# Performance work log

Hardware: AMD Instinct MI355X
Metric: run time of the kernel (lower is better)

The kernel has to match this reference:

```python
import jax, jax.numpy as jnp
import numpy as np

B, T, I, H, NC = 128, 256, 512, 1024, 1


def setup_inputs() -> dict:
    key = jax.random.key(0)
    ks = jax.random.split(key, 11)
    s = 1.0 / np.sqrt(H)  # torch nn.LSTM default init scale
    return {
        "x": jax.random.normal(ks[0], (B, T, I), jnp.float32),
        "W_ih0": jax.random.normal(ks[1], (4 * H, I), jnp.float32) * s,
        "W_hh0": jax.random.normal(ks[2], (4 * H, H), jnp.float32) * s,
        "b_ih0": jax.random.normal(ks[3], (4 * H,), jnp.float32) * s,
        "b_hh0": jax.random.normal(ks[4], (4 * H,), jnp.float32) * s,
        "W_ih1": jax.random.normal(ks[5], (4 * H, H), jnp.float32) * s,
        "W_hh1": jax.random.normal(ks[6], (4 * H, H), jnp.float32) * s,
        "b_ih1": jax.random.normal(ks[7], (4 * H,), jnp.float32) * s,
        "b_hh1": jax.random.normal(ks[8], (4 * H,), jnp.float32) * s,
        "W_fc": jax.random.normal(ks[9], (NC, H), jnp.float32) * s,
        "b_fc": jax.random.normal(ks[10], (NC,), jnp.float32) * s,
    }


def _lstm_layer(x_seq, W_ih, W_hh, b_ih, b_hh):
    # x_seq: [B, T, F]; torch gate order: i, f, g, o along 4H axis.
    b, h = x_seq.shape[0], W_hh.shape[1]
    # Precompute input projections for all timesteps (one big GEMM).
    x_proj = jnp.einsum("btf,gf->btg", x_seq, W_ih) + b_ih + b_hh  # [B,T,4H]

    def step(carry, xg):
        hprev, cprev = carry
        gates = xg + hprev @ W_hh.T  # [B,4H]
        i, f, g, o = jnp.split(gates, 4, axis=-1)
        c = jax.nn.sigmoid(f) * cprev + jax.nn.sigmoid(i) * jnp.tanh(g)
        hnew = jax.nn.sigmoid(o) * jnp.tanh(c)
        return (hnew, c), hnew

    init = (jnp.zeros((b, h), x_seq.dtype), jnp.zeros((b, h), x_seq.dtype))
    _, hs = jax.lax.scan(step, init, jnp.swapaxes(x_proj, 0, 1))  # [T,B,H]
    return jnp.swapaxes(hs, 0, 1)  # [B,T,H]


def reference(x, W_ih0, W_hh0, b_ih0, b_hh0, W_ih1, W_hh1, b_ih1, b_hh1, W_fc, b_fc):
    h1 = _lstm_layer(x, W_ih0, W_hh0, b_ih0, b_hh0)
    h2 = _lstm_layer(h1, W_ih1, W_hh1, b_ih1, b_hh1)
    return h2[:, -1, :] @ W_fc.T + b_fc  # [B, num_classes]
```

## Files before the change

kernel.cpp:

```cpp
#include <hip/hip_runtime.h>
#include <math.h>

typedef _Float16 half_t;
typedef _Float16 half8 __attribute__((ext_vector_type(8)));
typedef float f32x4 __attribute__((ext_vector_type(4)));
typedef unsigned long long u64;

#define B_ 128
#define T_ 256
#define I_ 512
#define H_ 1024

#define mfma16 __builtin_amdgcn_mfma_f32_16x16x32_f16

__global__ void k_convert_x(const float* __restrict__ x, half_t* __restrict__ x16, int n8) {
    int i = blockIdx.x * blockDim.x + threadIdx.x;
    if (i >= n8) return;
    const float4* xv = (const float4*)x;
    float4 a = xv[2 * i], b = xv[2 * i + 1];
    half8 o;
    o[0] = (half_t)a.x; o[1] = (half_t)a.y; o[2] = (half_t)a.z; o[3] = (half_t)a.w;
    o[4] = (half_t)b.x; o[5] = (half_t)b.y; o[6] = (half_t)b.z; o[7] = (half_t)b.w;
    int e = i * 8;
    int k = e & (I_ - 1);
    int t = (e >> 9) & (T_ - 1);
    int row = e >> 17;
    ((half8*)x16)[(((size_t)t * B_ + row) * I_ + k) >> 3] = o;
}

__global__ void k_pack_w(const float* __restrict__ Wih, const float* __restrict__ Whh,
                         half_t* __restrict__ out, int Kx, int Ktot) {
    int idx = blockIdx.x * blockDim.x + threadIdx.x;
    int total = 4096 * Ktot;
    if (idx >= total) return;
    int j = idx & 7;
    int lane = (idx >> 3) & 63;
    int nt = (idx >> 9) & 1;
    int rest = idx >> 10;
    int nkb = Ktot >> 5;
    int kb = rest % nkb;
    int hg = rest / nkb;
    int nl = nt * 16 + (lane & 15);
    int gate = nl >> 3, hoff = nl & 7;
    int row = gate * 1024 + hg * 8 + hoff;
    int k = kb * 32 + (lane >> 4) * 8 + j;
    float v = (k < Kx) ? Wih[(size_t)row * Kx + k] : Whh[(size_t)row * 1024 + (k - Kx)];
    out[idx] = (half_t)v;
}

__global__ void k_pack_bias(const float* __restrict__ bih, const float* __restrict__ bhh,
                            float* __restrict__ out) {
    int idx = blockIdx.x * blockDim.x + threadIdx.x;
    if (idx >= 4096) return;
    int hg = idx >> 5, c = idx & 31;
    int gate = c >> 3, hoff = c & 7;
    int row = gate * 1024 + hg * 8 + hoff;
    out[idx] = bih[row] + bhh[row];
}

__global__ void k_zero(unsigned int* __restrict__ p, int n) {
    int i = blockIdx.x * blockDim.x + threadIdx.x;
    if (i < n) p[i] = 0u;
}

__device__ __forceinline__ u64 sysld64(const half_t* p) {
    return __hip_atomic_load((const u64*)p, __ATOMIC_RELAXED, __HIP_MEMORY_SCOPE_SYSTEM);
}
__device__ __forceinline__ void sysst128(half_t* p, half8 v) {
    asm volatile("global_store_dwordx4 %0, %1, off sc0 sc1"
                 :: "v"(p), "v"(v) : "memory");
}
union H8U { half8 h; u64 u[2]; };

__device__ __forceinline__ void block_wait_all(const unsigned* f, unsigned tgt) {
    if (threadIdx.x < 64) {
        int lane = threadIdx.x;
        int gd = 0;
        for (;;) {
            unsigned a = __hip_atomic_load(f + lane, __ATOMIC_RELAXED,
                                           __HIP_MEMORY_SCOPE_SYSTEM);
            unsigned b = __hip_atomic_load(f + 64 + lane, __ATOMIC_RELAXED,
                                           __HIP_MEMORY_SCOPE_SYSTEM);
            if (__all((int)(a >= tgt && b >= tgt))) break;
            __builtin_amdgcn_s_sleep(4);
            if (++gd > (1 << 15)) break;
        }
    }
    __syncthreads();
    asm volatile("" ::: "memory");
}

template <int KX, bool LAY1, bool H2SEQ>
__device__ void run_layer(const half_t* __restrict__ srcX,
                          half_t* hA, half_t* hB,
                          const half_t* __restrict__ Wp, const float* __restrict__ biasp,
                          unsigned* flagsPre, unsigned* flagsOwn,
                          int rg, int cg, float* gacc, half_t* hstage)
{
    constexpr int KTOT = KX + 1024;
    constexpr int NKB  = KTOT >> 5;
    constexpr int NI_X = KX >> 8;
    constexpr int NI_H = 4;
    constexpr int NI   = NI_X + NI_H;

    const int tid = threadIdx.x;
    const int ks = tid >> 6, lane = tid & 63;
    const int q = lane >> 4, ml = lane & 15;
    const int hg = cg;
    const int r0 = rg * 32;

    half8 Breg[NI][2];
    {
        const half8* Wp8 = (const half8*)Wp;
        size_t base = (size_t)hg * NKB * 128 + lane;
#pragma unroll
        for (int i = 0; i < NI; ++i) {
            int kb = (i < NI_X) ? (NI_X * ks + i) : (KX / 32 + 4 * ks + (i - NI_X));
            Breg[i][0] = Wp8[base + (size_t)kb * 128];
            Breg[i][1] = Wp8[base + (size_t)kb * 128 + 64];
        }
#pragma unroll
        for (int i = 0; i < NI; ++i)
            asm volatile("" : "+v"(Breg[i][0]), "+v"(Breg[i][1]));
    }

    const int erow = tid >> 3, ehoff = tid & 7;
    float bi = 0.f, bf = 0.f, bgc = 0.f, bo = 0.f;
    if (tid < 256) {
        bi  = biasp[hg * 32 + 0 + ehoff];
        bf  = biasp[hg * 32 + 8 + ehoff];
        bgc = biasp[hg * 32 + 16 + ehoff];
        bo  = biasp[hg * 32 + 24 + ehoff];
    }
    float c_reg = 0.f;

    const unsigned* fpre = flagsPre + rg * 128;
    const unsigned* fown = flagsOwn + rg * 128;
    unsigned* myFlag = flagsOwn + rg * 128 + cg;

    for (int t = 0; t < T_; ++t) {
        f32x4 acc[2][2];
        acc[0][0] = (f32x4)0.f; acc[0][1] = (f32x4)0.f;
        acc[1][0] = (f32x4)0.f; acc[1][1] = (f32x4)0.f;

        if constexpr (LAY1) block_wait_all(fpre, (unsigned)(t + 1));
        const int t1 = LAY1 ? (t + 1) : t;
#pragma unroll
        for (int i = 0; i < NI_X; ++i) {
            int kg = 32 * (NI_X * ks + i) + q * 8;
#pragma unroll
            for (int rt = 0; rt < 2; ++rt) {
                int grow = r0 + rt * 16 + ml;
                half8 a = *(const half8*)(srcX + ((size_t)t1 * B_ + grow) * KX + kg);
                acc[rt][0] = mfma16(a, Breg[i][0], acc[rt][0], 0, 0, 0);
                acc[rt][1] = mfma16(a, Breg[i][1], acc[rt][1], 0, 0, 0);
            }
        }
        if (t > 0) block_wait_all(fown, (unsigned)t);
        const half_t* hp;
        if constexpr (!LAY1 || H2SEQ) hp = hA + (size_t)t * B_ * H_;
        else                          hp = (t & 1) ? hB : hA;
#pragma unroll
        for (int j = 0; j < NI_H; ++j) {
            int i = NI_X + j;
            int kh = 32 * (4 * ks + j) + q * 8;
#pragma unroll
            for (int rt = 0; rt < 2; ++rt) {
                int grow = r0 + rt * 16 + ml;
                half8 a;
                if constexpr (LAY1 && !H2SEQ) {
                    H8U u; const half_t* p = hp + (size_t)grow * H_ + kh;
                    u.u[0] = sysld64(p); u.u[1] = sysld64(p + 4);
                    a = u.h;
                } else {
                    a = *(const half8*)(hp + (size_t)grow * H_ + kh);
                }
                acc[rt][0] = mfma16(a, Breg[i][0], acc[rt][0], 0, 0, 0);
                acc[rt][1] = mfma16(a, Breg[i][1], acc[rt][1], 0, 0, 0);
            }
        }
#pragma unroll
        for (int rt = 0; rt < 2; ++rt)
#pragma unroll
            for (int ct = 0; ct < 2; ++ct)
#pragma unroll
                for (int r = 0; r < 4; ++r) {
                    int rl = rt * 16 + q * 4 + r;
                    int cl = ct * 16 + ml;
                    gacc[(ks * 32 + rl) * 32 + (cl ^ ((rl & 7) << 2))] = acc[rt][ct][r];
                }
        __syncthreads();
        if (tid < 256) {
            int swz = (erow & 7) << 2;
            float pi = 0.f, pf = 0.f, pg = 0.f, po = 0.f;
#pragma unroll
            for (int z = 0; z < 8; ++z) {
                const float* g = &gacc[(z * 32 + erow) * 32];
                pi += g[(0 + ehoff) ^ swz];
                pf += g[(8 + ehoff) ^ swz];
                pg += g[(16 + ehoff) ^ swz];
                po += g[(24 + ehoff) ^ swz];
            }
            pi += bi; pf += bf; pg += bgc; po += bo;
            float si = 1.f / (1.f + __expf(-pi));
            float sf = 1.f / (1.f + __expf(-pf));
            float so = 1.f / (1.f + __expf(-po));
            float tg = 1.f - 2.f / (__expf(2.f * pg) + 1.f);
            c_reg = sf * c_reg + si * tg;
            float th = 1.f - 2.f / (__expf(2.f * c_reg) + 1.f);
            float hn = so * th;
            hstage[erow * 8 + ehoff] = (half_t)hn;
        }
        __syncthreads();
        if (tid < 32) {
            half8 hv = *(const half8*)(hstage + tid * 8);
            half_t* dst;
            if constexpr (!LAY1 || H2SEQ)
                dst = hA + ((size_t)(t + 1) * B_ + (r0 + tid)) * H_ + hg * 8;
            else
                dst = ((t & 1) ? hA : hB) + (size_t)(r0 + tid) * H_ + hg * 8;
            sysst128(dst, hv);
        }
        if (tid == 0) {
            asm volatile("s_waitcnt vmcnt(0)" ::: "memory");
            __hip_atomic_store(myFlag, (unsigned)(t + 1),
                               __ATOMIC_RELAXED, __HIP_MEMORY_SCOPE_SYSTEM);
        }
    }
}

template <bool H2SEQ>
__launch_bounds__(512, 4)
__global__ void lstm_persist(const half_t* __restrict__ x16T, half_t* h1seq,
                             half_t* h2A, half_t* h2B,
                             const half_t* __restrict__ wp0, const half_t* __restrict__ wp1,
                             const float* __restrict__ bias0, const float* __restrict__ bias1,
                             unsigned* __restrict__ flags0, unsigned* __restrict__ flags1)
{
    __shared__ float gacc[8 * 32 * 32];
    __shared__ half_t hstage[32 * 8];
    int bid = blockIdx.x;
    int rg = bid & 3;
    int cg = bid >> 2;

    run_layer<512, false, true>(x16T, h1seq, (half_t*)0, wp0, bias0,
                                flags0, flags0, rg, cg, gacc, hstage);
    run_layer<1024, true, H2SEQ>(h1seq, h2A, h2B, wp1, bias1,
                                 flags0, flags1, rg, cg, gacc, hstage);
}

__global__ void k_fc(const half_t* __restrict__ h, const float* __restrict__ Wfc,
                     const float* __restrict__ bfc, float* __restrict__ out) {
    int m = blockIdx.x, lane = threadIdx.x;
    float s = 0.f;
    for (int k = lane; k < H_; k += 64) s += (float)h[m * H_ + k] * Wfc[k];
#pragma unroll
    for (int o = 32; o; o >>= 1) s += __shfl_down(s, o, 64);
    if (lane == 0) out[m] = s + bfc[0];
}

extern "C" void kernel_launch(void* const* d_in, const int* in_sizes, int n_in,
                              void* d_out, int out_size, void* d_ws, size_t ws_size,
                              hipStream_t stream) {
    const float* x    = (const float*)d_in[0];
    const float* Wih0 = (const float*)d_in[1];
    const float* Whh0 = (const float*)d_in[2];
    const float* bih0 = (const float*)d_in[3];
    const float* bhh0 = (const float*)d_in[4];
    const float* Wih1 = (const float*)d_in[5];
    const float* Whh1 = (const float*)d_in[6];
    const float* bih1 = (const float*)d_in[7];
    const float* bhh1 = (const float*)d_in[8];
    const float* Wfc  = (const float*)d_in[9];
    const float* bfc  = (const float*)d_in[10];
    float* out = (float*)d_out;

    char* ws = (char*)d_ws;
    size_t off = 0;
    auto carve = [&](size_t bytes) { void* p = ws + off; off += (bytes + 255) & ~(size_t)255; return p; };
    half_t* x16T   = (half_t*)carve((size_t)B_ * T_ * I_ * 2);
    half_t* h1seq  = (half_t*)carve((size_t)(T_ + 1) * B_ * H_ * 2);
    half_t* wp0    = (half_t*)carve((size_t)4096 * 1536 * 2);
    half_t* wp1    = (half_t*)carve((size_t)4096 * 2048 * 2);
    float*  bias0  = (float*)carve(4096 * 4);
    float*  bias1  = (float*)carve(4096 * 4);
    char*   states = (char*)carve(2 * (size_t)B_ * H_ * 2 + 8192);
    if (off > ws_size) return;

    half_t* h2a = (half_t*)states;
    half_t* h2b = h2a + B_ * H_;
    unsigned* flags0 = (unsigned*)(h2b + B_ * H_);
    unsigned* flags1 = flags0 + 512;

    half_t* h2seq = nullptr;
    if (off + (size_t)(T_ + 1) * B_ * H_ * 2 + 256 <= ws_size)
        h2seq = (half_t*)carve((size_t)(T_ + 1) * B_ * H_ * 2);

    k_convert_x<<<(B_ * T_ * I_ / 8 + 255) / 256, 256, 0, stream>>>(x, x16T, B_ * T_ * I_ / 8);
    k_pack_w<<<(4096 * 1536 + 255) / 256, 256, 0, stream>>>(Wih0, Whh0, wp0, 512, 1536);
    k_pack_w<<<(4096 * 2048 + 255) / 256, 256, 0, stream>>>(Wih1, Whh1, wp1, 1024, 2048);
    k_pack_bias<<<16, 256, 0, stream>>>(bih0, bhh0, bias0);
    k_pack_bias<<<16, 256, 0, stream>>>(bih1, bhh1, bias1);
    k_zero<<<(B_ * H_ / 2 + 255) / 256, 256, 0, stream>>>((unsigned int*)h1seq, B_ * H_ / 2);
    {
        int n = (2 * B_ * H_ * 2 + 8192) / 4;
        k_zero<<<(n + 255) / 256, 256, 0, stream>>>((unsigned int*)states, n);
    }
    if (h2seq)
        k_zero<<<(B_ * H_ / 2 + 255) / 256, 256, 0, stream>>>((unsigned int*)h2seq, B_ * H_ / 2);

    if (h2seq) {
        lstm_persist<true><<<dim3(512), dim3(512), 0, stream>>>(
            x16T, h1seq, h2seq, (half_t*)0, wp0, wp1, bias0, bias1, flags0, flags1);
        k_fc<<<128, 64, 0, stream>>>(h2seq + (size_t)T_ * B_ * H_, Wfc, bfc, out);
    } else {
        lstm_persist<false><<<dim3(512), dim3(512), 0, stream>>>(
            x16T, h1seq, h2a, h2b, wp0, wp1, bias0, bias1, flags0, flags1);
        k_fc<<<128, 64, 0, stream>>>(h2a, Wfc, bfc, out);
    }
}
```

Measured before the change: 4.333 ms.

## Run both LSTM layers concurrently on separate block sets with wavefront pipelining

Instead of every persistent block running layer 0 and then layer 1, half of the 512 blocks now own layer 0 and the other half own layer 1. Layer 1 consumes layer 0's hidden states one timestep behind through the existing flags, so the two recurrences overlap instead of running back to back. To keep the grid size, each block now covers 64 batch rows, processed as two 32-row halves, which doubles the LDS reduction buffer. The flag poll also switches to 128-bit loads over 32 lanes with a backoff sleep. The larger shared memory may reduce blocks per CU, and the co-residency needed for the spin-waits depends on that.

Result: slower. 7.016 ms (+61.9%).

```diff
diff --git a/kernel.cpp b/kernel.cpp
--- a/kernel.cpp
+++ b/kernel.cpp
@@ -4,6 +4,7 @@
 typedef _Float16 half_t;
 typedef _Float16 half8 __attribute__((ext_vector_type(8)));
 typedef float f32x4 __attribute__((ext_vector_type(4)));
+typedef unsigned int u32x4 __attribute__((ext_vector_type(4)));
 typedef unsigned long long u64;
 
 #define B_ 128
@@ -73,17 +74,19 @@
 union H8U { half8 h; u64 u[2]; };
 
 __device__ __forceinline__ void block_wait_all(const unsigned* f, unsigned tgt) {
-    if (threadIdx.x < 64) {
-        int lane = threadIdx.x;
+    if (threadIdx.x < 32) {
+        const unsigned* p = f + threadIdx.x * 4;
         int gd = 0;
         for (;;) {
-            unsigned a = __hip_atomic_load(f + lane, __ATOMIC_RELAXED,
-                                           __HIP_MEMORY_SCOPE_SYSTEM);
-            unsigned b = __hip_atomic_load(f + 64 + lane, __ATOMIC_RELAXED,
-                                           __HIP_MEMORY_SCOPE_SYSTEM);
-            if (__all((int)(a >= tgt && b >= tgt))) break;
-            __builtin_amdgcn_s_sleep(4);
-            if (++gd > (1 << 15)) break;
+            u32x4 v;
+            asm volatile("global_load_dwordx4 %0, %1, off sc0 sc1\n\t"
+                         "s_waitcnt vmcnt(0)"
+                         : "=v"(v) : "v"(p) : "memory");
+            if (__all((int)(v[0] >= tgt && v[1] >= tgt && v[2] >= tgt && v[3] >= tgt)))
+                break;
+            if (gd < 2) __builtin_amdgcn_s_sleep(4);
+            else        __builtin_amdgcn_s_sleep(16);
+            if (++gd > (1 << 14)) break;
         }
     }
     __syncthreads();
@@ -107,7 +110,7 @@
     const int ks = tid >> 6, lane = tid & 63;
     const int q = lane >> 4, ml = lane & 15;
     const int hg = cg;
-    const int r0 = rg * 32;
+    const int r0 = rg * 64;
 
     half8 Breg[NI][2];
     {
@@ -125,13 +128,10 @@
     }
 
     const int erow = tid >> 3, ehoff = tid & 7;
-    float bi = 0.f, bf = 0.f, bgc = 0.f, bo = 0.f;
-    if (tid < 256) {
-        bi  = biasp[hg * 32 + 0 + ehoff];
-        bf  = biasp[hg * 32 + 8 + ehoff];
-        bgc = biasp[hg * 32 + 16 + ehoff];
-        bo  = biasp[hg * 32 + 24 + ehoff];
-    }
+    const float bi  = biasp[hg * 32 + 0 + ehoff];
+    const float bf  = biasp[hg * 32 + 8 + ehoff];
+    const float bgc = biasp[hg * 32 + 16 + ehoff];
+    const float bo  = biasp[hg * 32 + 24 + ehoff];
     float c_reg = 0.f;
 
     const unsigned* fpre = flagsPre + rg * 128;
@@ -139,63 +139,68 @@
     unsigned* myFlag = flagsOwn + rg * 128 + cg;
 
     for (int t = 0; t < T_; ++t) {
-        f32x4 acc[2][2];
-        acc[0][0] = (f32x4)0.f; acc[0][1] = (f32x4)0.f;
-        acc[1][0] = (f32x4)0.f; acc[1][1] = (f32x4)0.f;
-
         if constexpr (LAY1) block_wait_all(fpre, (unsigned)(t + 1));
         const int t1 = LAY1 ? (t + 1) : t;
-#pragma unroll
-        for (int i = 0; i < NI_X; ++i) {
-            int kg = 32 * (NI_X * ks + i) + q * 8;
-#pragma unroll
-            for (int rt = 0; rt < 2; ++rt) {
-                int grow = r0 + rt * 16 + ml;
-                half8 a = *(const half8*)(srcX + ((size_t)t1 * B_ + grow) * KX + kg);
-                acc[rt][0] = mfma16(a, Breg[i][0], acc[rt][0], 0, 0, 0);
-                acc[rt][1] = mfma16(a, Breg[i][1], acc[rt][1], 0, 0, 0);
-            }
-        }
-        if (t > 0) block_wait_all(fown, (unsigned)t);
         const half_t* hp;
         if constexpr (!LAY1 || H2SEQ) hp = hA + (size_t)t * B_ * H_;
         else                          hp = (t & 1) ? hB : hA;
-#pragma unroll
-        for (int j = 0; j < NI_H; ++j) {
-            int i = NI_X + j;
-            int kh = 32 * (4 * ks + j) + q * 8;
-#pragma unroll
-            for (int rt = 0; rt < 2; ++rt) {
-                int grow = r0 + rt * 16 + ml;
-                half8 a;
-                if constexpr (LAY1 && !H2SEQ) {
-                    H8U u; const half_t* p = hp + (size_t)grow * H_ + kh;
-                    u.u[0] = sysld64(p); u.u[1] = sysld64(p + 4);
-                    a = u.h;
-                } else {
-                    a = *(const half8*)(hp + (size_t)grow * H_ + kh);
+
+#pragma unroll
+        for (int hf = 0; hf < 2; ++hf) {
+            const int rbase = r0 + hf * 32;
+            f32x4 acc[2][2];
+            acc[0][0] = (f32x4)0.f; acc[0][1] = (f32x4)0.f;
+            acc[1][0] = (f32x4)0.f; acc[1][1] = (f32x4)0.f;
+
+#pragma unroll
+            for (int i = 0; i < NI_X; ++i) {
+                int kg = 32 * (NI_X * ks + i) + q * 8;
+#pragma unroll
+                for (int rt = 0; rt < 2; ++rt) {
+                    int grow = rbase + rt * 16 + ml;
+                    half8 a = *(const half8*)(srcX + ((size_t)t1 * B_ + grow) * KX + kg);
+                    acc[rt][0] = mfma16(a, Breg[i][0], acc[rt][0], 0, 0, 0);
+                    acc[rt][1] = mfma16(a, Breg[i][1], acc[rt][1], 0, 0, 0);
                 }
-                acc[rt][0] = mfma16(a, Breg[i][0], acc[rt][0], 0, 0, 0);
-                acc[rt][1] = mfma16(a, Breg[i][1], acc[rt][1], 0, 0, 0);
             }
-        }
-#pragma unroll
-        for (int rt = 0; rt < 2; ++rt)
-#pragma unroll
-            for (int ct = 0; ct < 2; ++ct)
-#pragma unroll
-                for (int r = 0; r < 4; ++r) {
-                    int rl = rt * 16 + q * 4 + r;
-                    int cl = ct * 16 + ml;
-                    gacc[(ks * 32 + rl) * 32 + (cl ^ ((rl & 7) << 2))] = acc[rt][ct][r];
+            if (hf == 0 && t > 0) block_wait_all(fown, (unsigned)t);
+#pragma unroll
+            for (int j = 0; j < NI_H; ++j) {
+                int i = NI_X + j;
+                int kh = 32 * (4 * ks + j) + q * 8;
+#pragma unroll
+                for (int rt = 0; rt < 2; ++rt) {
+                    int grow = rbase + rt * 16 + ml;
+                    half8 a;
+                    if constexpr (LAY1 && !H2SEQ) {
+                        H8U u; const half_t* p = hp + (size_t)grow * H_ + kh;
+                        u.u[0] = sysld64(p); u.u[1] = sysld64(p + 4);
+                        a = u.h;
+                    } else {
+                        a = *(const half8*)(hp + (size_t)grow * H_ + kh);
+                    }
+                    acc[rt][0] = mfma16(a, Breg[i][0], acc[rt][0], 0, 0, 0);
+                    acc[rt][1] = mfma16(a, Breg[i][1], acc[rt][1], 0, 0, 0);
                 }
+            }
+#pragma unroll
+            for (int rt = 0; rt < 2; ++rt)
+#pragma unroll
+                for (int ct = 0; ct < 2; ++ct)
+#pragma unroll
+                    for (int r = 0; r < 4; ++r) {
+                        int rl = hf * 32 + rt * 16 + q * 4 + r;
+                        int cl = ct * 16 + ml;
+                        gacc[(ks * 64 + rl) * 32 + (cl ^ ((rl & 7) << 2))] = acc[rt][ct][r];
+                    }
+        }
         __syncthreads();
-        if (tid < 256) {
+        {
             int swz = (erow & 7) << 2;
             float pi = 0.f, pf = 0.f, pg = 0.f, po = 0.f;
 #pragma unroll
             for (int z = 0; z < 8; ++z) {
-                const float* g = &gacc[(z * 32 + erow) * 32];
+                const float* g = &gacc[(z * 64 + erow) * 32];
                 pi += g[(0 + ehoff) ^ swz];
                 pf += g[(8 + ehoff) ^ swz];
                 pg += g[(16 + ehoff) ^ swz];
@@ -212,7 +217,7 @@
             hstage[erow * 8 + ehoff] = (half_t)hn;
         }
         __syncthreads();
-        if (tid < 32) {
+        if (tid < 64) {
             half8 hv = *(const half8*)(hstage + tid * 8);
             half_t* dst;
             if constexpr (!LAY1 || H2SEQ)
@@ -237,16 +242,20 @@
                              const float* __restrict__ bias0, const float* __restrict__ bias1,
                              unsigned* __restrict__ flags0, unsigned* __restrict__ flags1)
 {
-    __shared__ float gacc[8 * 32 * 32];
-    __shared__ half_t hstage[32 * 8];
+    __shared__ float gacc[8 * 64 * 32];
+    __shared__ half_t hstage[64 * 8];
     int bid = blockIdx.x;
-    int rg = bid & 3;
-    int cg = bid >> 2;
-
-    run_layer<512, false, true>(x16T, h1seq, (half_t*)0, wp0, bias0,
-                                flags0, flags0, rg, cg, gacc, hstage);
-    run_layer<1024, true, H2SEQ>(h1seq, h2A, h2B, wp1, bias1,
-                                 flags0, flags1, rg, cg, gacc, hstage);
+    int lay = bid >> 8;
+    int u = bid & 255;
+    int rg = u & 1;
+    int cg = u >> 1;
+
+    if (lay == 0)
+        run_layer<512, false, true>(x16T, h1seq, (half_t*)0, wp0, bias0,
+                                    flags0, flags0, rg, cg, gacc, hstage);
+    else
+        run_layer<1024, true, H2SEQ>(h1seq, h2A, h2B, wp1, bias1,
+                                     flags0, flags1, rg, cg, gacc, hstage);
 }
 
 __global__ void k_fc(const half_t* __restrict__ h, const float* __restrict__ Wfc,
```

## Replace block-wide flag barrier with per-wave waits on chunk-spaced flags

Applied to the files above, without the earlier changes.

Replaces the block-level wait, where one wave polls 128 flags and then a __syncthreads follows, with a per-wave wait. Each wave polls only the flags for the k-slice of h it consumes, using four lanes doing dwordx4 system-coherent loads. Flags are spread into 1KB-separated chunks so they do not share cache lines, and the first retries use a shorter sleep. This removes the block barrier and cuts per-step polling latency in the recurrent loop. It costs a larger zeroed flag region, and correctness now depends on each wave seeing only the flags it needs.

Measured after the change: 4.594 ms. 6.0% more time.

```diff
diff --git a/kernel.cpp b/kernel.cpp
--- a/kernel.cpp
+++ b/kernel.cpp
@@ -4,6 +4,7 @@
 typedef _Float16 half_t;
 typedef _Float16 half8 __attribute__((ext_vector_type(8)));
 typedef float f32x4 __attribute__((ext_vector_type(4)));
+typedef unsigned int u32x4 __attribute__((ext_vector_type(4)));
 typedef unsigned long long u64;
 
 #define B_ 128
@@ -72,21 +73,23 @@
 }
 union H8U { half8 h; u64 u[2]; };
 
-__device__ __forceinline__ void block_wait_all(const unsigned* f, unsigned tgt) {
-    if (threadIdx.x < 64) {
-        int lane = threadIdx.x;
-        int gd = 0;
-        for (;;) {
-            unsigned a = __hip_atomic_load(f + lane, __ATOMIC_RELAXED,
-                                           __HIP_MEMORY_SCOPE_SYSTEM);
-            unsigned b = __hip_atomic_load(f + 64 + lane, __ATOMIC_RELAXED,
-                                           __HIP_MEMORY_SCOPE_SYSTEM);
-            if (__all((int)(a >= tgt && b >= tgt))) break;
-            __builtin_amdgcn_s_sleep(4);
-            if (++gd > (1 << 15)) break;
-        }
-    }
-    __syncthreads();
+#define CHUNK_U32 256
+__device__ __forceinline__ void wave_wait(const unsigned* chunk0, unsigned tgt) {
+    int lane = threadIdx.x & 63;
+    const unsigned* p = chunk0 + (lane & 3) * CHUNK_U32;
+    int gd = 0;
+    for (;;) {
+        u32x4 v; v[0] = tgt; v[1] = tgt; v[2] = tgt; v[3] = tgt;
+        if (lane < 4)
+            asm volatile("global_load_dwordx4 %0, %1, off sc0 sc1\n\t"
+                         "s_waitcnt vmcnt(0)"
+                         : "=v"(v) : "v"(p) : "memory");
+        if (__all((int)(v[0] >= tgt && v[1] >= tgt && v[2] >= tgt && v[3] >= tgt)))
+            break;
+        if (gd < 4) __builtin_amdgcn_s_sleep(1);
+        else        __builtin_amdgcn_s_sleep(4);
+        if (++gd > (1 << 15)) break;
+    }
     asm volatile("" ::: "memory");
 }
 
@@ -134,16 +137,16 @@
     }
     float c_reg = 0.f;
 
-    const unsigned* fpre = flagsPre + rg * 128;
-    const unsigned* fown = flagsOwn + rg * 128;
-    unsigned* myFlag = flagsOwn + rg * 128 + cg;
+    const unsigned* preC = flagsPre + rg * 8192 + (4 * ks) * CHUNK_U32;
+    const unsigned* ownC = flagsOwn + rg * 8192 + (4 * ks) * CHUNK_U32;
+    unsigned* myFlag = flagsOwn + rg * 8192 + (cg >> 2) * CHUNK_U32 + (cg & 3);
 
     for (int t = 0; t < T_; ++t) {
         f32x4 acc[2][2];
         acc[0][0] = (f32x4)0.f; acc[0][1] = (f32x4)0.f;
         acc[1][0] = (f32x4)0.f; acc[1][1] = (f32x4)0.f;
 
-        if constexpr (LAY1) block_wait_all(fpre, (unsigned)(t + 1));
+        if constexpr (LAY1) wave_wait(preC, (unsigned)(t + 1));
         const int t1 = LAY1 ? (t + 1) : t;
 #pragma unroll
         for (int i = 0; i < NI_X; ++i) {
@@ -156,7 +159,7 @@
                 acc[rt][1] = mfma16(a, Breg[i][1], acc[rt][1], 0, 0, 0);
             }
         }
-        if (t > 0) block_wait_all(fown, (unsigned)t);
+        if (t > 0) wave_wait(ownC, (unsigned)t);
         const half_t* hp;
         if constexpr (!LAY1 || H2SEQ) hp = hA + (size_t)t * B_ * H_;
         else                          hp = (t & 1) ? hB : hA;
@@ -284,13 +287,13 @@
     half_t* wp1    = (half_t*)carve((size_t)4096 * 2048 * 2);
     float*  bias0  = (float*)carve(4096 * 4);
     float*  bias1  = (float*)carve(4096 * 4);
-    char*   states = (char*)carve(2 * (size_t)B_ * H_ * 2 + 8192);
+    char*   states = (char*)carve(2 * (size_t)B_ * H_ * 2 + 262144 + 256);
     if (off > ws_size) return;
 
     half_t* h2a = (half_t*)states;
     half_t* h2b = h2a + B_ * H_;
     unsigned* flags0 = (unsigned*)(h2b + B_ * H_);
-    unsigned* flags1 = flags0 + 512;
+    unsigned* flags1 = flags0 + 4 * 8192;
 
     half_t* h2seq = nullptr;
     if (off + (size_t)(T_ + 1) * B_ * H_ * 2 + 256 <= ws_size)
@@ -303,7 +306,7 @@
     k_pack_bias<<<16, 256, 0, stream>>>(bih1, bhh1, bias1);
     k_zero<<<(B_ * H_ / 2 + 255) / 256, 256, 0, stream>>>((unsigned int*)h1seq, B_ * H_ / 2);
     {
-        int n = (2 * B_ * H_ * 2 + 8192) / 4;
+        int n = (2 * B_ * H_ * 2 + 262144 + 256) / 4;
         k_zero<<<(n + 255) / 256, 256, 0, stream>>>((unsigned int*)states, n);
     }
     if (h2seq)
```
